# Kernel tuning notes

Hardware: AMD Instinct MI355X
Metric: run time of the kernel (lower is better)

Reference implementation:

```python
import jax, jax.numpy as jnp
import numpy as np
import math

B, T = 16, 512
P = 256          # num_memory_positions
E = 128          # embedding_dim
NB = 4           # num_beings
K = 4            # attention_radius
TEMP = 8.0       # attention_temperature
PHI = 1.618033988749895


def setup_inputs() -> dict:
    key = jax.random.key(0)
    ks = jax.random.split(key, 8)
    x = jax.random.normal(ks[0], (B, T, 8), jnp.float32)
    W_in = jax.random.normal(ks[1], (8, E), jnp.float32) * 0.1
    b_in = jnp.zeros((E,), jnp.float32)
    W_out = jax.random.normal(ks[2], (E, 8), jnp.float32) * 0.1
    b_out = jnp.zeros((8,), jnp.float32)
    W_p = jax.random.normal(ks[3], (E, E), jnp.float32) * (1.0 / np.sqrt(E))
    b_p = jnp.zeros((E,), jnp.float32)
    ptr_dest = jax.random.uniform(ks[4], (NB, P), jnp.float32) * P
    jump_W = jax.random.normal(ks[5], (NB, E), jnp.float32) * 0.1
    jump_b = jnp.zeros((NB,), jnp.float32)
    ctx_strength = jnp.full((NB,), 0.2, jnp.float32)
    pe = np.zeros((NB, E), np.float32)
    for i in range(NB):
        ph = i * PHI
        v = []
        for h in range(1, 9):
            v += [math.sin(h * ph), math.cos(h * ph)]
        pe[i, :16] = v  # phase_embedding padded with zeros to E (E >= 16)
    phase_bias = jnp.asarray(pe)
    seg = P / NB
    pointer_init = jax.random.uniform(ks[6], (NB, B), jnp.float32) * seg + jnp.arange(NB, dtype=jnp.float32)[:, None] * seg
    return dict(x=x, W_in=W_in, b_in=b_in, W_out=W_out, b_out=b_out,
                W_p=W_p, b_p=b_p, ptr_dest=ptr_dest, jump_W=jump_W,
                jump_b=jump_b, ctx_strength=ctx_strength,
                phase_bias=phase_bias, pointer_init=pointer_init)


def _forward(x, W_in, b_in, W_out, b_out, W_p, b_p, ptr_dest, jump_W,
             jump_b, ctx_strength, phase_bias, pointer_init):
    offsets = jnp.arange(-K, K + 1)          # [W]
    b_ix = jnp.arange(B)                     # [B]
    half = P / 2.0
    ring0 = jnp.zeros((B, P, E), x.dtype)
    hid0 = jnp.zeros((NB, B, E), x.dtype)

    def step(carry, x_t):
        ring, ptrs, hids = carry
        inp = x_t @ W_in + b_in              # [B,E]
        outs, new_ptrs, new_hids = [], [], []
        for i in range(NB):                  # beings sequential (share ring)
            ptr, hid = ptrs[i], hids[i]
            base = jnp.clip(jnp.floor(ptr).astype(jnp.int32), 0, P - 1)
            idx = (base[:, None] + offsets[None, :]) % P            # [B,W]
            delta = jnp.mod(idx.astype(x_t.dtype) - ptr[:, None] + half, P) - half
            w = jax.nn.softmax(-(delta ** 2) / TEMP, axis=1)         # [B,W]
            nbhd = ring[b_ix[:, None], idx]                          # [B,W,E]
            ctx = jnp.sum(w[..., None] * nbhd, axis=1)               # [B,E]
            comb = inp + jax.nn.sigmoid(ctx_strength[i]) * ctx + 0.1 * phase_bias[i]
            s = jnp.tanh(comb + hid)
            s = jnp.tanh(s @ W_p + b_p)      # depth-1 = 1 processing layer
            ring = ring.at[b_ix[:, None], idx].add(w[..., None] * s[:, None, :])
            cur = jnp.clip(ptr.astype(jnp.int32), 0, P - 1)
            jump_target = ptr_dest[i][cur]                           # [B]
            probs = jax.nn.sigmoid(s @ jump_W[i] + jump_b[i])        # [B]
            hard = (probs > 0.5).astype(s.dtype)
            should_jump = hard - jax.lax.stop_gradient(probs) + probs
            walk = (ptr + 1.0) % P
            new_ptrs.append(jnp.where(should_jump > 0.5, jump_target, walk))
            new_hids.append(s)
            outs.append(s @ W_out + b_out)                           # [B,8]
        out_t = jnp.mean(jnp.stack(outs), axis=0)                    # [B,8] (training-mode mean)
        return (ring, jnp.stack(new_ptrs), jnp.stack(new_hids)), out_t

    _, ys = jax.lax.scan(step, (ring0, pointer_init, hid0), jnp.swapaxes(x, 0, 1))
    return jnp.swapaxes(ys, 0, 1)            # [B,T,8]


def reference(x, W_in, b_in, W_out, b_out, W_p, b_p, ptr_dest, jump_W,
              jump_b, ctx_strength, phase_bias, pointer_init):
    return _forward(x, W_in, b_in, W_out, b_out, W_p, b_p, ptr_dest,
                    jump_W, jump_b, ctx_strength, phase_bias, pointer_init)
```

## Files before the change

### kernel.cpp

```cpp
#include <hip/hip_runtime.h>
#include <cmath>

namespace {
constexpr int B_ = 16, T_ = 512, P_ = 256, E_ = 128, NB_ = 4, K_ = 4;

__device__ __forceinline__ float rcpf(float x) { return __builtin_amdgcn_rcpf(x); }
__device__ __forceinline__ float fast_tanh(float x) {
    float a = fabsf(x);
    float t = __expf(-2.0f * a);
    float r = 1.0f - 2.0f * t * rcpf(1.0f + t);
    return copysignf(r, x);
}
__device__ __forceinline__ float redkq(float v) {
    v += __shfl_xor(v, 16);
    v += __shfl_xor(v, 32);
    return v;
}
__device__ __forceinline__ float sel4(int kq, float a, float b, float c, float d) {
    const float t0 = (kq & 1) ? b : a;
    const float t1 = (kq & 1) ? d : c;
    return (kq & 2) ? t1 : t0;
}
}

__global__ __launch_bounds__(256, 1)
void swarm_ring_kernel(const float* __restrict__ x,
                       const float* __restrict__ W_in,
                       const float* __restrict__ b_in,
                       const float* __restrict__ W_out,
                       const float* __restrict__ b_out,
                       const float* __restrict__ W_p,
                       const float* __restrict__ b_p,
                       const float* __restrict__ ptr_dest,
                       const float* __restrict__ jump_W,
                       const float* __restrict__ jump_b,
                       const float* __restrict__ ctx_strength,
                       const float* __restrict__ phase_bias,
                       const float* __restrict__ pointer_init,
                       float* __restrict__ out)
{
    __shared__ alignas(16) float ring[P_ * E_];
    __shared__ alignas(16) float s1p[NB_ * E_];
    __shared__ alignas(16) float red[16];
    __shared__ alignas(16) float hist[16][132];
    __shared__ alignas(16) float wout_s[8][132];

    const int tid = threadIdx.x;
    const int b   = blockIdx.x;
    const int w   = tid >> 6;
    const int l   = tid & 63;
    const int sub = l & 15;
    const int kq  = l >> 4;
    const int e0  = ((w << 4) | sub) << 1;

    for (int k4 = tid; k4 < P_ * E_ / 4; k4 += 256)
        ((float4*)ring)[k4] = make_float4(0.f, 0.f, 0.f, 0.f);
    for (int idx = tid; idx < 8 * E_; idx += 256) {
        const int m = idx >> 7, ee = idx & 127;
        wout_s[m][ee] = W_out[ee * 8 + m] * 0.25f;
    }

    float2 wp2[32];
    #pragma unroll
    for (int kk = 0; kk < 32; ++kk)
        wp2[kk] = *(const float2*)(W_p + (kq * 32 + kk) * E_ + e0);

    const float2 bin2 = *(const float2*)(b_in + e0);
    const float2 bp2  = *(const float2*)(b_p + e0);
    const float  bout_m = b_out[tid & 7];

    float2 pb2[NB_], jw2[NB_], hid2[NB_];
    float  sigc[NB_], jb_r[NB_], ptrv[NB_];
    #pragma unroll
    for (int i = 0; i < NB_; ++i) {
        const float2 pb = *(const float2*)(phase_bias + i * E_ + e0);
        pb2[i] = make_float2(0.1f * pb.x, 0.1f * pb.y);
        jw2[i] = *(const float2*)(jump_W + i * E_ + e0);
        sigc[i] = 1.0f / (1.0f + __expf(-ctx_strength[i]));
        jb_r[i] = jump_b[i];
        hid2[i] = make_float2(0.f, 0.f);
        ptrv[i] = pointer_init[i * B_ + b];
    }

    const float* xb = x + (size_t)b * T_ * 8;
    float xt[8];
    {
        float4 a0 = ((const float4*)xb)[0], a1 = ((const float4*)xb)[1];
        xt[0]=a0.x; xt[1]=a0.y; xt[2]=a0.z; xt[3]=a0.w;
        xt[4]=a1.x; xt[5]=a1.y; xt[6]=a1.z; xt[7]=a1.w;
    }

    const float Cw1 = 0.8824969f, Cw2 = 0.60653066f, Cw3 = 0.32465247f, Cw4 = 0.13533528f;
    const float Dw1 = 0.7788008f, Dw2 = 0.36787944f, Dw3 = 0.105399225f, Dw4 = 0.018315639f;

    __syncthreads();

    for (int t = 0; t < T_; ++t) {
        int   baseA[NB_];
        float fA[NB_], psinv[NB_], jt[NB_], wgt[NB_][9];
        #pragma unroll
        for (int i = 0; i < NB_; ++i) {
            const float p = ptrv[i];
            const int base = (int)p;
            baseA[i] = base;
            jt[i] = ptr_dest[i * P_ + base];
            const float f = p - (float)base;
            fA[i] = f;
            const float r  = __expf(0.25f * f);
            const float r2 = r * r, r3 = r2 * r, r4 = r2 * r2;
            const float ri = rcpf(r), ri2 = ri * ri, ri3 = ri2 * ri, ri4 = ri2 * ri2;
            const float p0 = Cw4*ri4, p1 = Cw3*ri3, p2 = Cw2*ri2, p3 = Cw1*ri, p4 = 1.0f,
                        p5 = Cw1*r,  p6 = Cw2*r2,  p7 = Cw3*r3,  p8 = Cw4*r4;
            const float sum = ((p0+p1)+(p2+p3)) + ((p4+p5)+(p6+p7)) + p8;
            const float inv = rcpf(sum);
            psinv[i] = inv;
            wgt[i][0]=p0*inv; wgt[i][1]=p1*inv; wgt[i][2]=p2*inv; wgt[i][3]=p3*inv;
            wgt[i][4]=p4*inv; wgt[i][5]=p5*inv; wgt[i][6]=p6*inv; wgt[i][7]=p7*inv;
            wgt[i][8]=p8*inv;
        }

        int ddm[NB_][NB_];
        int lev[NB_];
        lev[0] = 0;
        #pragma unroll
        for (int j = 1; j < NB_; ++j) {
            int mx = -1;
            #pragma unroll
            for (int i = 0; i < j; ++i) {
                const int dd = ((baseA[j] - baseA[i] + 128) & 255) - 128;
                ddm[j][i] = dd;
                if (dd >= -8 && dd <= 8 && lev[i] > mx) mx = lev[i];
            }
            lev[j] = mx + 1;
        }
        const int nlev = 1 + ((lev[1] > lev[0] ? lev[1] : lev[0]) > (lev[2] > lev[3] ? lev[2] : lev[3])
                              ? (lev[1] > lev[0] ? lev[1] : lev[0])
                              : (lev[2] > lev[3] ? lev[2] : lev[3]));

        float  ws0[NB_], ws1[NB_];
        float2 ctxp2[NB_];
        #pragma unroll
        for (int i = 0; i < NB_; ++i) {
            ws0[i] = sel4(kq, wgt[i][0], wgt[i][1], wgt[i][2], wgt[i][3]);
            ws1[i] = sel4(kq, wgt[i][4], wgt[i][5], wgt[i][6], wgt[i][7]);
            const int r0 = (baseA[i] + kq - K_) & (P_ - 1);
            const int r1 = (baseA[i] + kq + 4 - K_) & (P_ - 1);
            const float2 g0 = *(const float2*)(ring + r0 * E_ + e0);
            const float2 g1 = *(const float2*)(ring + r1 * E_ + e0);
            float cx = fmaf(ws1[i], g1.x, ws0[i] * g0.x);
            float cy = fmaf(ws1[i], g1.y, ws0[i] * g0.y);
            if (kq == 0) {
                const int r2 = (baseA[i] + 8 - K_) & (P_ - 1);
                const float2 g2 = *(const float2*)(ring + r2 * E_ + e0);
                cx = fmaf(wgt[i][8], g2.x, cx);
                cy = fmaf(wgt[i][8], g2.y, cy);
            }
            ctxp2[i] = make_float2(redkq(cx), redkq(cy));
        }

        float coefm[NB_][NB_];
        #pragma unroll
        for (int j = 1; j < NB_; ++j) {
            #pragma unroll
            for (int i = 0; i < j; ++i) {
                const int dd = ddm[j][i];
                float c = 0.f;
                if (dd >= -8 && dd <= 8) {
                    const float A = (float)dd - fA[i];
                    const float s  = __expf(-0.25f * (A - fA[j]));
                    const float G  = __expf(0.125f * (fA[i] * fA[i] - A * A));
                    const float s2p = s * s, s3p = s2p * s, s4p = s2p * s2p;
                    const float si = rcpf(s), si2 = si * si, si3 = si2 * si, si4 = si2 * si2;
                    float acc = 0.f;
                    acc += (dd >= 0)              ? Dw4 * si4 : 0.f;
                    acc += (dd >= -1 && dd <= 7)  ? Dw3 * si3 : 0.f;
                    acc += (dd >= -2 && dd <= 6)  ? Dw2 * si2 : 0.f;
                    acc += (dd >= -3 && dd <= 5)  ? Dw1 * si  : 0.f;
                    acc += (dd >= -4 && dd <= 4)  ? 1.0f      : 0.f;
                    acc += (dd >= -5 && dd <= 3)  ? Dw1 * s   : 0.f;
                    acc += (dd >= -6 && dd <= 2)  ? Dw2 * s2p : 0.f;
                    acc += (dd >= -7 && dd <= 1)  ? Dw3 * s3p : 0.f;
                    acc += (dd <= 0)              ? Dw4 * s4p : 0.f;
                    c = psinv[i] * psinv[j] * G * acc;
                }
                coefm[j][i] = c;
            }
        }

        float2 inp2 = bin2;
        #pragma unroll
        for (int k = 0; k < 8; ++k) {
            const float2 wk = *(const float2*)(W_in + k * E_ + e0);
            inp2.x = fmaf(xt[k], wk.x, inp2.x);
            inp2.y = fmaf(xt[k], wk.y, inp2.y);
        }

        float xtn[8];
        if (t + 1 < T_) {
            float4 a0 = ((const float4*)(xb + (t + 1) * 8))[0];
            float4 a1 = ((const float4*)(xb + (t + 1) * 8))[1];
            xtn[0]=a0.x; xtn[1]=a0.y; xtn[2]=a0.z; xtn[3]=a0.w;
            xtn[4]=a1.x; xtn[5]=a1.y; xtn[6]=a1.z; xtn[7]=a1.w;
        } else {
            #pragma unroll
            for (int k = 0; k < 8; ++k) xtn[k] = 0.f;
        }

        float2 sv2[NB_];
        #pragma unroll
        for (int j = 0; j < NB_; ++j) sv2[j] = make_float2(0.f, 0.f);

        for (int L = 0; L < nlev; ++L) {
            #pragma unroll
            for (int j = 0; j < NB_; ++j) {
                if (lev[j] != L) continue;
                float2 ctx = ctxp2[j];
                #pragma unroll
                for (int i = 0; i < j; ++i) {
                    ctx.x = fmaf(coefm[j][i], sv2[i].x, ctx.x);
                    ctx.y = fmaf(coefm[j][i], sv2[i].y, ctx.y);
                }
                float2 s1;
                s1.x = fast_tanh(fmaf(sigc[j], ctx.x, inp2.x + pb2[j].x + hid2[j].x));
                s1.y = fast_tanh(fmaf(sigc[j], ctx.y, inp2.y + pb2[j].y + hid2[j].y));
                if (kq == 0) *(float2*)(s1p + j * E_ + e0) = s1;
            }
            __syncthreads();

            #pragma unroll
            for (int j = 0; j < NB_; ++j) {
                if (lev[j] != L) continue;
                const float4* sp = (const float4*)(s1p + j * E_) + kq * 8;
                float ax = 0.f, ay = 0.f;
                #pragma unroll
                for (int kk = 0; kk < 8; ++kk) {
                    const float4 sq = sp[kk];
                    const float2 wa = wp2[4 * kk + 0], wb = wp2[4 * kk + 1];
                    const float2 wc = wp2[4 * kk + 2], wd = wp2[4 * kk + 3];
                    ax = fmaf(sq.x, wa.x, ax); ay = fmaf(sq.x, wa.y, ay);
                    ax = fmaf(sq.y, wb.x, ax); ay = fmaf(sq.y, wb.y, ay);
                    ax = fmaf(sq.z, wc.x, ax); ay = fmaf(sq.z, wc.y, ay);
                    ax = fmaf(sq.w, wd.x, ax); ay = fmaf(sq.w, wd.y, ay);
                }
                float2 s2;
                s2.x = fast_tanh(redkq(ax) + bp2.x);
                s2.y = fast_tanh(redkq(ay) + bp2.y);
                sv2[j] = s2; hid2[j] = s2;

                const int r0 = (baseA[j] + kq - K_) & (P_ - 1);
                float2* q0 = (float2*)(ring + r0 * E_ + e0);
                float2 v0 = *q0;
                v0.x = fmaf(ws0[j], s2.x, v0.x); v0.y = fmaf(ws0[j], s2.y, v0.y);
                *q0 = v0;
                const int r1 = (baseA[j] + kq + 4 - K_) & (P_ - 1);
                float2* q1 = (float2*)(ring + r1 * E_ + e0);
                float2 v1 = *q1;
                v1.x = fmaf(ws1[j], s2.x, v1.x); v1.y = fmaf(ws1[j], s2.y, v1.y);
                *q1 = v1;
                if (kq == 0) {
                    const int r2 = (baseA[j] + 8 - K_) & (P_ - 1);
                    float2* q2 = (float2*)(ring + r2 * E_ + e0);
                    float2 v2 = *q2;
                    v2.x = fmaf(wgt[j][8], s2.x, v2.x); v2.y = fmaf(wgt[j][8], s2.y, v2.y);
                    *q2 = v2;
                }
            }
        }

        {
            float vj0 = fmaf(sv2[0].y, jw2[0].y, sv2[0].x * jw2[0].x);
            float vj1 = fmaf(sv2[1].y, jw2[1].y, sv2[1].x * jw2[1].x);
            float vj2 = fmaf(sv2[2].y, jw2[2].y, sv2[2].x * jw2[2].x);
            float vj3 = fmaf(sv2[3].y, jw2[3].y, sv2[3].x * jw2[3].x);
            #pragma unroll
            for (int off = 1; off < 16; off <<= 1) {
                vj0 += __shfl_xor(vj0, off);
                vj1 += __shfl_xor(vj1, off);
                vj2 += __shfl_xor(vj2, off);
                vj3 += __shfl_xor(vj3, off);
            }
            if (l == 0)
                ((float4*)red)[w] = make_float4(vj0, vj1, vj2, vj3);
        }

        {
            float2 ssum2;
            ssum2.x = (sv2[0].x + sv2[1].x) + (sv2[2].x + sv2[3].x);
            ssum2.y = (sv2[0].y + sv2[1].y) + (sv2[2].y + sv2[3].y);
            if (kq == 0) *(float2*)(&hist[t & 15][e0]) = ssum2;
        }

        __syncthreads();

        {
            const float4 r0 = ((const float4*)red)[0];
            const float4 r1 = ((const float4*)red)[1];
            const float4 r2 = ((const float4*)red)[2];
            const float4 r3 = ((const float4*)red)[3];
            const float zz[4] = {
                ((r0.x + r1.x) + (r2.x + r3.x)) + jb_r[0],
                ((r0.y + r1.y) + (r2.y + r3.y)) + jb_r[1],
                ((r0.z + r1.z) + (r2.z + r3.z)) + jb_r[2],
                ((r0.w + r1.w) + (r2.w + r3.w)) + jb_r[3]};
            #pragma unroll
            for (int i = 0; i < NB_; ++i) {
                float np;
                if (zz[i] > 0.0f) np = jt[i];
                else { np = ptrv[i] + 1.0f; if (np >= 256.0f) np -= 256.0f; }
                ptrv[i] = np;
            }
        }

        if ((t & 7) == 7 && tid < 64) {
            const int tt = tid >> 3;
            const int m  = tid & 7;
            const float* hrow = hist[(t - 7 + tt) & 15];
            const float* wrow = wout_s[m];
            float acc = 0.f;
            #pragma unroll
            for (int q = 0; q < 32; ++q) {
                const float4 h4 = ((const float4*)hrow)[q];
                const float4 w4 = ((const float4*)wrow)[q];
                acc += ((h4.x * w4.x + h4.y * w4.y) + (h4.z * w4.z + h4.w * w4.w));
            }
            out[((size_t)b * T_ + (t - 7 + tt)) * 8 + m] = acc + bout_m;
        }

        #pragma unroll
        for (int k = 0; k < 8; ++k) xt[k] = xtn[k];
    }
}

extern "C" void kernel_launch(void* const* d_in, const int* in_sizes, int n_in,
                              void* d_out, int out_size, void* d_ws, size_t ws_size,
                              hipStream_t stream) {
    (void)in_sizes; (void)n_in; (void)out_size; (void)d_ws; (void)ws_size;
    swarm_ring_kernel<<<dim3(B_), dim3(256), 0, stream>>>(
        (const float*)d_in[0],  (const float*)d_in[1],  (const float*)d_in[2],
        (const float*)d_in[3],  (const float*)d_in[4],  (const float*)d_in[5],
        (const float*)d_in[6],  (const float*)d_in[7],  (const float*)d_in[8],
        (const float*)d_in[9],  (const float*)d_in[10], (const float*)d_in[11],
        (const float*)d_in[12], (float*)d_out);
}
```

Before: 2.060 ms.

## Add helper wavefront that speculatively precomputes next-step pointer geometry for both branches

```diff
diff --git a/kernel.cpp b/kernel.cpp
--- a/kernel.cpp
+++ b/kernel.cpp
@@ -3,6 +3,8 @@
 
 namespace {
 constexpr int B_ = 16, T_ = 512, P_ = 256, E_ = 128, NB_ = 4, K_ = 4;
+constexpr float Cw1 = 0.8824969f, Cw2 = 0.60653066f, Cw3 = 0.32465247f, Cw4 = 0.13533528f;
+constexpr float Dw1 = 0.7788008f, Dw2 = 0.36787944f, Dw3 = 0.105399225f, Dw4 = 0.018315639f;
 
 __device__ __forceinline__ float rcpf(float x) { return __builtin_amdgcn_rcpf(x); }
 __device__ __forceinline__ float fast_tanh(float x) {
@@ -21,9 +23,46 @@
     const float t1 = (kq & 1) ? d : c;
     return (kq & 2) ? t1 : t0;
 }
-}
-
-__global__ __launch_bounds__(256, 1)
+__device__ __forceinline__ void mk_geo(float p, int& base, float& f, float& ps, float* wgt) {
+    base = (int)p;
+    f = p - (float)base;
+    const float r  = __expf(0.25f * f);
+    const float r2 = r * r, r3 = r2 * r, r4 = r2 * r2;
+    const float ri = rcpf(r), ri2 = ri * ri, ri3 = ri2 * ri, ri4 = ri2 * ri2;
+    const float p0 = Cw4*ri4, p1 = Cw3*ri3, p2 = Cw2*ri2, p3 = Cw1*ri, p4 = 1.0f,
+                p5 = Cw1*r,  p6 = Cw2*r2,  p7 = Cw3*r3,  p8 = Cw4*r4;
+    const float sum = ((p0+p1)+(p2+p3)) + ((p4+p5)+(p6+p7)) + p8;
+    const float inv = rcpf(sum);
+    ps = inv;
+    wgt[0]=p0*inv; wgt[1]=p1*inv; wgt[2]=p2*inv; wgt[3]=p3*inv; wgt[4]=p4*inv;
+    wgt[5]=p5*inv; wgt[6]=p6*inv; wgt[7]=p7*inv; wgt[8]=p8*inv;
+}
+__device__ __forceinline__ float mk_coef(int bj, int bi, float fj, float fi, float psj, float psi) {
+    const int dd = ((bj - bi + 128) & 255) - 128;
+    float c = 0.f;
+    if (dd >= -8 && dd <= 8) {
+        const float A = (float)dd - fi;
+        const float s  = __expf(-0.25f * (A - fj));
+        const float G  = __expf(0.125f * (fi * fi - A * A));
+        const float s2p = s * s, s3p = s2p * s, s4p = s2p * s2p;
+        const float si = rcpf(s), si2 = si * si, si3 = si2 * si, si4 = si2 * si2;
+        float acc = 0.f;
+        acc += (dd >= 0)              ? Dw4 * si4 : 0.f;
+        acc += (dd >= -1 && dd <= 7)  ? Dw3 * si3 : 0.f;
+        acc += (dd >= -2 && dd <= 6)  ? Dw2 * si2 : 0.f;
+        acc += (dd >= -3 && dd <= 5)  ? Dw1 * si  : 0.f;
+        acc += (dd >= -4 && dd <= 4)  ? 1.0f      : 0.f;
+        acc += (dd >= -5 && dd <= 3)  ? Dw1 * s   : 0.f;
+        acc += (dd >= -6 && dd <= 2)  ? Dw2 * s2p : 0.f;
+        acc += (dd >= -7 && dd <= 1)  ? Dw3 * s3p : 0.f;
+        acc += (dd <= 0)              ? Dw4 * s4p : 0.f;
+        c = psi * psj * G * acc;
+    }
+    return c;
+}
+}
+
+__global__ __launch_bounds__(320, 1)
 void swarm_ring_kernel(const float* __restrict__ x,
                        const float* __restrict__ W_in,
                        const float* __restrict__ b_in,
@@ -44,18 +83,21 @@
     __shared__ alignas(16) float red[16];
     __shared__ alignas(16) float hist[16][132];
     __shared__ alignas(16) float wout_s[8][132];
+    __shared__ alignas(16) float geoL[2][2][NB_][12];
+    __shared__ alignas(16) float coefL[2][2][2][6];
 
     const int tid = threadIdx.x;
     const int b   = blockIdx.x;
     const int w   = tid >> 6;
     const int l   = tid & 63;
+    const bool isMain = (w < 4);
     const int sub = l & 15;
     const int kq  = l >> 4;
-    const int e0  = ((w << 4) | sub) << 1;
-
-    for (int k4 = tid; k4 < P_ * E_ / 4; k4 += 256)
+    const int e0  = (((w & 3) << 4) | sub) << 1;
+
+    for (int k4 = tid; k4 < P_ * E_ / 4; k4 += 320)
         ((float4*)ring)[k4] = make_float4(0.f, 0.f, 0.f, 0.f);
-    for (int idx = tid; idx < 8 * E_; idx += 256) {
+    for (int idx = tid; idx < 8 * E_; idx += 320) {
         const int m = idx >> 7, ee = idx & 127;
         wout_s[m][ee] = W_out[ee * 8 + m] * 0.25f;
     }
@@ -70,7 +112,7 @@
     const float  bout_m = b_out[tid & 7];
 
     float2 pb2[NB_], jw2[NB_], hid2[NB_];
-    float  sigc[NB_], jb_r[NB_], ptrv[NB_];
+    float  sigc[NB_], jb_r[NB_];
     #pragma unroll
     for (int i = 0; i < NB_; ++i) {
         const float2 pb = *(const float2*)(phase_bias + i * E_ + e0);
@@ -79,47 +121,103 @@
         sigc[i] = 1.0f / (1.0f + __expf(-ctx_strength[i]));
         jb_r[i] = jump_b[i];
         hid2[i] = make_float2(0.f, 0.f);
-        ptrv[i] = pointer_init[i * B_ + b];
+    }
+
+    float pc[2][NB_], jtc[2][NB_];
+    int   bc[2][NB_];
+
+    if (w == 4) {
+        float fb[NB_], pbs[NB_];
+        int   bb[NB_];
+        #pragma unroll
+        for (int i = 0; i < NB_; ++i) {
+            const float p = pointer_init[i * B_ + b];
+            int bs; float f, ps, wg[9];
+            mk_geo(p, bs, f, ps, wg);
+            fb[i] = f; pbs[i] = ps; bb[i] = bs;
+            pc[0][i] = pc[1][i] = p;
+            bc[0][i] = bc[1][i] = bs;
+            const float jt = ptr_dest[i * P_ + bs];
+            jtc[0][i] = jtc[1][i] = jt;
+            if (l == 0) {
+                #pragma unroll
+                for (int c = 0; c < 2; ++c) {
+                    float* gw = &geoL[0][c][i][0];
+                    #pragma unroll
+                    for (int o = 0; o < 9; ++o) gw[o] = wg[o];
+                    gw[9] = __int_as_float(bs);
+                }
+            }
+        }
+        if (l == 0) {
+            int p = 0;
+            #pragma unroll
+            for (int j = 1; j < NB_; ++j)
+                #pragma unroll
+                for (int i = 0; i < j; ++i) {
+                    const float c = mk_coef(bb[j], bb[i], fb[j], fb[i], pbs[j], pbs[i]);
+                    coefL[0][0][0][p] = c; coefL[0][0][1][p] = c;
+                    coefL[0][1][0][p] = c; coefL[0][1][1][p] = c;
+                    ++p;
+                }
+        }
     }
 
     const float* xb = x + (size_t)b * T_ * 8;
     float xt[8];
-    {
+    if (isMain) {
         float4 a0 = ((const float4*)xb)[0], a1 = ((const float4*)xb)[1];
         xt[0]=a0.x; xt[1]=a0.y; xt[2]=a0.z; xt[3]=a0.w;
         xt[4]=a1.x; xt[5]=a1.y; xt[6]=a1.z; xt[7]=a1.w;
     }
 
-    const float Cw1 = 0.8824969f, Cw2 = 0.60653066f, Cw3 = 0.32465247f, Cw4 = 0.13533528f;
-    const float Dw1 = 0.7788008f, Dw2 = 0.36787944f, Dw3 = 0.105399225f, Dw4 = 0.018315639f;
-
     __syncthreads();
 
     for (int t = 0; t < T_; ++t) {
-        int   baseA[NB_];
-        float fA[NB_], psinv[NB_], jt[NB_], wgt[NB_][9];
-        #pragma unroll
-        for (int i = 0; i < NB_; ++i) {
-            const float p = ptrv[i];
-            const int base = (int)p;
-            baseA[i] = base;
-            jt[i] = ptr_dest[i * P_ + base];
-            const float f = p - (float)base;
-            fA[i] = f;
-            const float r  = __expf(0.25f * f);
-            const float r2 = r * r, r3 = r2 * r, r4 = r2 * r2;
-            const float ri = rcpf(r), ri2 = ri * ri, ri3 = ri2 * ri, ri4 = ri2 * ri2;
-            const float p0 = Cw4*ri4, p1 = Cw3*ri3, p2 = Cw2*ri2, p3 = Cw1*ri, p4 = 1.0f,
-                        p5 = Cw1*r,  p6 = Cw2*r2,  p7 = Cw3*r3,  p8 = Cw4*r4;
-            const float sum = ((p0+p1)+(p2+p3)) + ((p4+p5)+(p6+p7)) + p8;
-            const float inv = rcpf(sum);
-            psinv[i] = inv;
-            wgt[i][0]=p0*inv; wgt[i][1]=p1*inv; wgt[i][2]=p2*inv; wgt[i][3]=p3*inv;
-            wgt[i][4]=p4*inv; wgt[i][5]=p5*inv; wgt[i][6]=p6*inv; wgt[i][7]=p7*inv;
-            wgt[i][8]=p8*inv;
-        }
-
-        int ddm[NB_][NB_];
+        int jm[NB_];
+        if (t == 0) {
+            #pragma unroll
+            for (int i = 0; i < NB_; ++i) jm[i] = 0;
+        } else {
+            const float4 r0 = ((const float4*)red)[0];
+            const float4 r1 = ((const float4*)red)[1];
+            const float4 r2 = ((const float4*)red)[2];
+            const float4 r3 = ((const float4*)red)[3];
+            jm[0] = (((r0.x + r1.x) + (r2.x + r3.x)) + jb_r[0]) > 0.f;
+            jm[1] = (((r0.y + r1.y) + (r2.y + r3.y)) + jb_r[1]) > 0.f;
+            jm[2] = (((r0.z + r1.z) + (r2.z + r3.z)) + jb_r[2]) > 0.f;
+            jm[3] = (((r0.w + r1.w) + (r2.w + r3.w)) + jb_r[3]) > 0.f;
+        }
+        const int buf = t & 1;
+
+        int   base[NB_];
+        float wgt[NB_][9];
+        float coefm[6];
+        if (isMain) {
+            #pragma unroll
+            for (int i = 0; i < NB_; ++i) {
+                const float4* gp = (const float4*)&geoL[buf][jm[i]][i][0];
+                const float4 ga = gp[0], gb = gp[1], gc = gp[2];
+                wgt[i][0]=ga.x; wgt[i][1]=ga.y; wgt[i][2]=ga.z; wgt[i][3]=ga.w;
+                wgt[i][4]=gb.x; wgt[i][5]=gb.y; wgt[i][6]=gb.z; wgt[i][7]=gb.w;
+                wgt[i][8]=gc.x;
+                base[i] = __float_as_int(gc.y);
+            }
+            {
+                int p = 0;
+                #pragma unroll
+                for (int j = 1; j < NB_; ++j)
+                    #pragma unroll
+                    for (int i = 0; i < j; ++i) {
+                        coefm[p] = coefL[buf][jm[i]][jm[j]][p];
+                        ++p;
+                    }
+            }
+        } else {
+            #pragma unroll
+            for (int i = 0; i < NB_; ++i) base[i] = jm[i] ? bc[1][i] : bc[0][i];
+        }
+
         int lev[NB_];
         lev[0] = 0;
         #pragma unroll
@@ -127,83 +225,101 @@
             int mx = -1;
             #pragma unroll
             for (int i = 0; i < j; ++i) {
-                const int dd = ((baseA[j] - baseA[i] + 128) & 255) - 128;
-                ddm[j][i] = dd;
+                const int dd = ((base[j] - base[i] + 128) & 255) - 128;
                 if (dd >= -8 && dd <= 8 && lev[i] > mx) mx = lev[i];
             }
             lev[j] = mx + 1;
         }
-        const int nlev = 1 + ((lev[1] > lev[0] ? lev[1] : lev[0]) > (lev[2] > lev[3] ? lev[2] : lev[3])
-                              ? (lev[1] > lev[0] ? lev[1] : lev[0])
-                              : (lev[2] > lev[3] ? lev[2] : lev[3]));
+        const int m01 = lev[1] > lev[0] ? lev[1] : lev[0];
+        const int m23 = lev[2] > lev[3] ? lev[2] : lev[3];
+        const int nlev = 1 + (m01 > m23 ? m01 : m23);
+
+        if (w == 4 && t + 1 < T_) {
+            float pt[NB_], jtt[NB_];
+            #pragma unroll
+            for (int i = 0; i < NB_; ++i) {
+                pt[i]  = jm[i] ? pc[1][i]  : pc[0][i];
+                jtt[i] = jm[i] ? jtc[1][i] : jtc[0][i];
+            }
+            float fC[2][NB_], psC[2][NB_];
+            #pragma unroll
+            for (int c = 0; c < 2; ++c) {
+                #pragma unroll
+                for (int i = 0; i < NB_; ++i) {
+                    float p;
+                    if (c == 0) { p = pt[i] + 1.0f; if (p >= 256.0f) p -= 256.0f; }
+                    else        { p = jtt[i]; }
+                    int bs; float f, ps, wg[9];
+                    mk_geo(p, bs, f, ps, wg);
+                    fC[c][i] = f; psC[c][i] = ps;
+                    pc[c][i] = p; bc[c][i] = bs;
+                    jtc[c][i] = ptr_dest[i * P_ + bs];
+                    if (l == 0) {
+                        float* gw = &geoL[buf ^ 1][c][i][0];
+                        #pragma unroll
+                        for (int o = 0; o < 9; ++o) gw[o] = wg[o];
+                        gw[9] = __int_as_float(bs);
+                    }
+                }
+            }
+            if (l == 0) {
+                #pragma unroll
+                for (int cj = 0; cj < 2; ++cj)
+                    #pragma unroll
+                    for (int ci = 0; ci < 2; ++ci) {
+                        int p = 0;
+                        #pragma unroll
+                        for (int j = 1; j < NB_; ++j)
+                            #pragma unroll
+                            for (int i = 0; i < j; ++i) {
+                                coefL[buf ^ 1][ci][cj][p] =
+                                    mk_coef(bc[cj][j], bc[ci][i], fC[cj][j], fC[ci][i],
+                                            psC[cj][j], psC[ci][i]);
+                                ++p;
+                            }
+                    }
+            }
+        }
 
         float  ws0[NB_], ws1[NB_];
         float2 ctxp2[NB_];
-        #pragma unroll
-        for (int i = 0; i < NB_; ++i) {
-            ws0[i] = sel4(kq, wgt[i][0], wgt[i][1], wgt[i][2], wgt[i][3]);
-            ws1[i] = sel4(kq, wgt[i][4], wgt[i][5], wgt[i][6], wgt[i][7]);
-            const int r0 = (baseA[i] + kq - K_) & (P_ - 1);
-            const int r1 = (baseA[i] + kq + 4 - K_) & (P_ - 1);
-            const float2 g0 = *(const float2*)(ring + r0 * E_ + e0);
-            const float2 g1 = *(const float2*)(ring + r1 * E_ + e0);
-            float cx = fmaf(ws1[i], g1.x, ws0[i] * g0.x);
-            float cy = fmaf(ws1[i], g1.y, ws0[i] * g0.y);
-            if (kq == 0) {
-                const int r2 = (baseA[i] + 8 - K_) & (P_ - 1);
-                const float2 g2 = *(const float2*)(ring + r2 * E_ + e0);
-                cx = fmaf(wgt[i][8], g2.x, cx);
-                cy = fmaf(wgt[i][8], g2.y, cy);
-            }
-            ctxp2[i] = make_float2(redkq(cx), redkq(cy));
-        }
-
-        float coefm[NB_][NB_];
-        #pragma unroll
-        for (int j = 1; j < NB_; ++j) {
-            #pragma unroll
-            for (int i = 0; i < j; ++i) {
-                const int dd = ddm[j][i];
-                float c = 0.f;
-                if (dd >= -8 && dd <= 8) {
-                    const float A = (float)dd - fA[i];
-                    const float s  = __expf(-0.25f * (A - fA[j]));
-                    const float G  = __expf(0.125f * (fA[i] * fA[i] - A * A));
-                    const float s2p = s * s, s3p = s2p * s, s4p = s2p * s2p;
-                    const float si = rcpf(s), si2 = si * si, si3 = si2 * si, si4 = si2 * si2;
-                    float acc = 0.f;
-                    acc += (dd >= 0)              ? Dw4 * si4 : 0.f;
-                    acc += (dd >= -1 && dd <= 7)  ? Dw3 * si3 : 0.f;
-                    acc += (dd >= -2 && dd <= 6)  ? Dw2 * si2 : 0.f;
-                    acc += (dd >= -3 && dd <= 5)  ? Dw1 * si  : 0.f;
-                    acc += (dd >= -4 && dd <= 4)  ? 1.0f      : 0.f;
-                    acc += (dd >= -5 && dd <= 3)  ? Dw1 * s   : 0.f;
-                    acc += (dd >= -6 && dd <= 2)  ? Dw2 * s2p : 0.f;
-                    acc += (dd >= -7 && dd <= 1)  ? Dw3 * s3p : 0.f;
-                    acc += (dd <= 0)              ? Dw4 * s4p : 0.f;
-                    c = psinv[i] * psinv[j] * G * acc;
-                }
-                coefm[j][i] = c;
-            }
-        }
-
-        float2 inp2 = bin2;
-        #pragma unroll
-        for (int k = 0; k < 8; ++k) {
-            const float2 wk = *(const float2*)(W_in + k * E_ + e0);
-            inp2.x = fmaf(xt[k], wk.x, inp2.x);
-            inp2.y = fmaf(xt[k], wk.y, inp2.y);
-        }
-
-        float xtn[8];
-        if (t + 1 < T_) {
-            float4 a0 = ((const float4*)(xb + (t + 1) * 8))[0];
-            float4 a1 = ((const float4*)(xb + (t + 1) * 8))[1];
-            xtn[0]=a0.x; xtn[1]=a0.y; xtn[2]=a0.z; xtn[3]=a0.w;
-            xtn[4]=a1.x; xtn[5]=a1.y; xtn[6]=a1.z; xtn[7]=a1.w;
-        } else {
-            #pragma unroll
-            for (int k = 0; k < 8; ++k) xtn[k] = 0.f;
+        float2 inp2;
+        float  xtn[8];
+        if (isMain) {
+            #pragma unroll
+            for (int i = 0; i < NB_; ++i) {
+                ws0[i] = sel4(kq, wgt[i][0], wgt[i][1], wgt[i][2], wgt[i][3]);
+                ws1[i] = sel4(kq, wgt[i][4], wgt[i][5], wgt[i][6], wgt[i][7]);
+                const int r0 = (base[i] + kq - K_) & (P_ - 1);
+                const int r1 = (base[i] + kq + 4 - K_) & (P_ - 1);
+                const float2 g0 = *(const float2*)(ring + r0 * E_ + e0);
+                const float2 g1 = *(const float2*)(ring + r1 * E_ + e0);
+                float cx = fmaf(ws1[i], g1.x, ws0[i] * g0.x);
+                float cy = fmaf(ws1[i], g1.y, ws0[i] * g0.y);
+                if (kq == 0) {
+                    const int r2 = (base[i] + 8 - K_) & (P_ - 1);
+                    const float2 g2 = *(const float2*)(ring + r2 * E_ + e0);
+                    cx = fmaf(wgt[i][8], g2.x, cx);
+                    cy = fmaf(wgt[i][8], g2.y, cy);
+                }
+                ctxp2[i] = make_float2(redkq(cx), redkq(cy));
+            }
+            inp2 = bin2;
+            #pragma unroll
+            for (int k = 0; k < 8; ++k) {
+                const float2 wk = *(const float2*)(W_in + k * E_ + e0);
+                inp2.x = fmaf(xt[k], wk.x, inp2.x);
+                inp2.y = fmaf(xt[k], wk.y, inp2.y);
+            }
+            if (t + 1 < T_) {
+                float4 a0 = ((const float4*)(xb + (t + 1) * 8))[0];
+                float4 a1 = ((const float4*)(xb + (t + 1) * 8))[1];
+                xtn[0]=a0.x; xtn[1]=a0.y; xtn[2]=a0.z; xtn[3]=a0.w;
+                xtn[4]=a1.x; xtn[5]=a1.y; xtn[6]=a1.z; xtn[7]=a1.w;
+            } else {
+                #pragma unroll
+                for (int k = 0; k < 8; ++k) xtn[k] = 0.f;
+            }
         }
 
         float2 sv2[NB_];
@@ -211,63 +327,67 @@
         for (int j = 0; j < NB_; ++j) sv2[j] = make_float2(0.f, 0.f);
 
         for (int L = 0; L < nlev; ++L) {
-            #pragma unroll
-            for (int j = 0; j < NB_; ++j) {
-                if (lev[j] != L) continue;
-                float2 ctx = ctxp2[j];
-                #pragma unroll
-                for (int i = 0; i < j; ++i) {
-                    ctx.x = fmaf(coefm[j][i], sv2[i].x, ctx.x);
-                    ctx.y = fmaf(coefm[j][i], sv2[i].y, ctx.y);
-                }
-                float2 s1;
-                s1.x = fast_tanh(fmaf(sigc[j], ctx.x, inp2.x + pb2[j].x + hid2[j].x));
-                s1.y = fast_tanh(fmaf(sigc[j], ctx.y, inp2.y + pb2[j].y + hid2[j].y));
-                if (kq == 0) *(float2*)(s1p + j * E_ + e0) = s1;
+            if (isMain) {
+                #pragma unroll
+                for (int j = 0; j < NB_; ++j) {
+                    if (lev[j] != L) continue;
+                    float2 ctx = ctxp2[j];
+                    #pragma unroll
+                    for (int i = 0; i < j; ++i) {
+                        const float c = coefm[j * (j - 1) / 2 + i];
+                        ctx.x = fmaf(c, sv2[i].x, ctx.x);
+                        ctx.y = fmaf(c, sv2[i].y, ctx.y);
+                    }
+                    float2 s1;
+                    s1.x = fast_tanh(fmaf(sigc[j], ctx.x, inp2.x + pb2[j].x + hid2[j].x));
+                    s1.y = fast_tanh(fmaf(sigc[j], ctx.y, inp2.y + pb2[j].y + hid2[j].y));
+                    if (kq == 0) *(float2*)(s1p + j * E_ + e0) = s1;
+                }
             }
             __syncthreads();
-
-            #pragma unroll
-            for (int j = 0; j < NB_; ++j) {
-                if (lev[j] != L) continue;
-                const float4* sp = (const float4*)(s1p + j * E_) + kq * 8;
-                float ax = 0.f, ay = 0.f;
-                #pragma unroll
-                for (int kk = 0; kk < 8; ++kk) {
-                    const float4 sq = sp[kk];
-                    const float2 wa = wp2[4 * kk + 0], wb = wp2[4 * kk + 1];
-                    const float2 wc = wp2[4 * kk + 2], wd = wp2[4 * kk + 3];
-                    ax = fmaf(sq.x, wa.x, ax); ay = fmaf(sq.x, wa.y, ay);
-                    ax = fmaf(sq.y, wb.x, ax); ay = fmaf(sq.y, wb.y, ay);
-                    ax = fmaf(sq.z, wc.x, ax); ay = fmaf(sq.z, wc.y, ay);
-                    ax = fmaf(sq.w, wd.x, ax); ay = fmaf(sq.w, wd.y, ay);
-                }
-                float2 s2;
-                s2.x = fast_tanh(redkq(ax) + bp2.x);
-                s2.y = fast_tanh(redkq(ay) + bp2.y);
-                sv2[j] = s2; hid2[j] = s2;
-
-                const int r0 = (baseA[j] + kq - K_) & (P_ - 1);
-                float2* q0 = (float2*)(ring + r0 * E_ + e0);
-                float2 v0 = *q0;
-                v0.x = fmaf(ws0[j], s2.x, v0.x); v0.y = fmaf(ws0[j], s2.y, v0.y);
-                *q0 = v0;
-                const int r1 = (baseA[j] + kq + 4 - K_) & (P_ - 1);
-                float2* q1 = (float2*)(ring + r1 * E_ + e0);
-                float2 v1 = *q1;
-                v1.x = fmaf(ws1[j], s2.x, v1.x); v1.y = fmaf(ws1[j], s2.y, v1.y);
-                *q1 = v1;
-                if (kq == 0) {
-                    const int r2 = (baseA[j] + 8 - K_) & (P_ - 1);
-                    float2* q2 = (float2*)(ring + r2 * E_ + e0);
-                    float2 v2 = *q2;
-                    v2.x = fmaf(wgt[j][8], s2.x, v2.x); v2.y = fmaf(wgt[j][8], s2.y, v2.y);
-                    *q2 = v2;
-                }
-            }
-        }
-
-        {
+            if (isMain) {
+                #pragma unroll
+                for (int j = 0; j < NB_; ++j) {
+                    if (lev[j] != L) continue;
+                    const float4* sp = (const float4*)(s1p + j * E_) + kq * 8;
+                    float ax = 0.f, ay = 0.f;
+                    #pragma unroll
+                    for (int kk = 0; kk < 8; ++kk) {
+                        const float4 sq = sp[kk];
+                        const float2 wa = wp2[4 * kk + 0], wb = wp2[4 * kk + 1];
+                        const float2 wc = wp2[4 * kk + 2], wd = wp2[4 * kk + 3];
+                        ax = fmaf(sq.x, wa.x, ax); ay = fmaf(sq.x, wa.y, ay);
+                        ax = fmaf(sq.y, wb.x, ax); ay = fmaf(sq.y, wb.y, ay);
+                        ax = fmaf(sq.z, wc.x, ax); ay = fmaf(sq.z, wc.y, ay);
+                        ax = fmaf(sq.w, wd.x, ax); ay = fmaf(sq.w, wd.y, ay);
+                    }
+                    float2 s2v;
+                    s2v.x = fast_tanh(redkq(ax) + bp2.x);
+                    s2v.y = fast_tanh(redkq(ay) + bp2.y);
+                    sv2[j] = s2v; hid2[j] = s2v;
+
+                    const int r0 = (base[j] + kq - K_) & (P_ - 1);
+                    float2* q0 = (float2*)(ring + r0 * E_ + e0);
+                    float2 v0 = *q0;
+                    v0.x = fmaf(ws0[j], s2v.x, v0.x); v0.y = fmaf(ws0[j], s2v.y, v0.y);
+                    *q0 = v0;
+                    const int r1 = (base[j] + kq + 4 - K_) & (P_ - 1);
+                    float2* q1 = (float2*)(ring + r1 * E_ + e0);
+                    float2 v1 = *q1;
+                    v1.x = fmaf(ws1[j], s2v.x, v1.x); v1.y = fmaf(ws1[j], s2v.y, v1.y);
+                    *q1 = v1;
+                    if (kq == 0) {
+                        const int r2 = (base[j] + 8 - K_) & (P_ - 1);
+                        float2* q2 = (float2*)(ring + r2 * E_ + e0);
+                        float2 v2 = *q2;
+                        v2.x = fmaf(wgt[j][8], s2v.x, v2.x); v2.y = fmaf(wgt[j][8], s2v.y, v2.y);
+                        *q2 = v2;
+                    }
+                }
+            }
+        }
+
+        if (isMain) {
             float vj0 = fmaf(sv2[0].y, jw2[0].y, sv2[0].x * jw2[0].x);
             float vj1 = fmaf(sv2[1].y, jw2[1].y, sv2[1].x * jw2[1].x);
             float vj2 = fmaf(sv2[2].y, jw2[2].y, sv2[2].x * jw2[2].x);
@@ -281,9 +401,7 @@
             }
             if (l == 0)
                 ((float4*)red)[w] = make_float4(vj0, vj1, vj2, vj3);
-        }
-
-        {
+
             float2 ssum2;
             ssum2.x = (sv2[0].x + sv2[1].x) + (sv2[2].x + sv2[3].x);
             ssum2.y = (sv2[0].y + sv2[1].y) + (sv2[2].y + sv2[3].y);
@@ -291,25 +409,6 @@
         }
 
         __syncthreads();
-
-        {
-            const float4 r0 = ((const float4*)red)[0];
-            const float4 r1 = ((const float4*)red)[1];
-            const float4 r2 = ((const float4*)red)[2];
-            const float4 r3 = ((const float4*)red)[3];
-            const float zz[4] = {
-                ((r0.x + r1.x) + (r2.x + r3.x)) + jb_r[0],
-                ((r0.y + r1.y) + (r2.y + r3.y)) + jb_r[1],
-                ((r0.z + r1.z) + (r2.z + r3.z)) + jb_r[2],
-                ((r0.w + r1.w) + (r2.w + r3.w)) + jb_r[3]};
-            #pragma unroll
-            for (int i = 0; i < NB_; ++i) {
-                float np;
-                if (zz[i] > 0.0f) np = jt[i];
-                else { np = ptrv[i] + 1.0f; if (np >= 256.0f) np -= 256.0f; }
-                ptrv[i] = np;
-            }
-        }
 
         if ((t & 7) == 7 && tid < 64) {
             const int tt = tid >> 3;
@@ -326,8 +425,10 @@
             out[((size_t)b * T_ + (t - 7 + tt)) * 8 + m] = acc + bout_m;
         }
 
-        #pragma unroll
-        for (int k = 0; k < 8; ++k) xt[k] = xtn[k];
+        if (isMain) {
+            #pragma unroll
+            for (int k = 0; k < 8; ++k) xt[k] = xtn[k];
+        }
     }
 }
 
@@ -335,7 +436,7 @@
                               void* d_out, int out_size, void* d_ws, size_t ws_size,
                               hipStream_t stream) {
     (void)in_sizes; (void)n_in; (void)out_size; (void)d_ws; (void)ws_size;
-    swarm_ring_kernel<<<dim3(B_), dim3(256), 0, stream>>>(
+    swarm_ring_kernel<<<dim3(B_), dim3(320), 0, stream>>>(
         (const float*)d_in[0],  (const float*)d_in[1],  (const float*)d_in[2],
         (const float*)d_in[3],  (const float*)d_in[4],  (const float*)d_in[5],
         (const float*)d_in[6],  (const float*)d_in[7],  (const float*)d_in[8],
```

Result: slower. 3.250 ms (+57.8%).
